# Kernel optimization log

Measured on AMD Instinct MI355X. Metric: run time of the kernel, lower is better.

The kernel has to match this reference:

```python
import jax, jax.numpy as jnp
import numpy as np

INPUT_DIM = 1024
HIDDEN_DIM = 2048
NUM_BLOCKS = 8
BLOCK_SIZE = HIDDEN_DIM // NUM_BLOCKS
BATCH = 2048


def setup_inputs() -> dict:
    key = jax.random.key(0)
    ks = jax.random.split(key, 6)
    # PyTorch GRUCell init: uniform(-1/sqrt(hidden_size), 1/sqrt(hidden_size))
    bound = 1.0 / np.sqrt(BLOCK_SIZE)
    u = lambda k, shape: jax.random.uniform(k, shape, jnp.float32, -bound, bound)
    return {
        "input": jax.random.normal(ks[0], (BATCH, INPUT_DIM), jnp.float32),
        "hidden": jax.random.normal(ks[1], (BATCH, HIDDEN_DIM), jnp.float32),
        # stacked per-block GRUCell params (block-diagonal structure)
        "W_ih": u(ks[2], (NUM_BLOCKS, 3 * BLOCK_SIZE, INPUT_DIM)),
        "W_hh": u(ks[3], (NUM_BLOCKS, 3 * BLOCK_SIZE, BLOCK_SIZE)),
        "b_ih": u(ks[4], (NUM_BLOCKS, 3 * BLOCK_SIZE)),
        "b_hh": u(ks[5], (NUM_BLOCKS, 3 * BLOCK_SIZE)),
    }


def reference(input, hidden, W_ih, W_hh, b_ih, b_hh):
    B = input.shape[0]
    nb, g3, bs = W_hh.shape  # [num_blocks, 3*block_size, block_size]
    hb = hidden.reshape(B, nb, bs)                      # [B, nb, bs]
    # input-to-gate and hidden-to-gate projections, batched over blocks
    gi = jnp.einsum("bi,ngi->bng", input, W_ih) + b_ih  # [B, nb, 3*bs]
    gh = jnp.einsum("bns,ngs->bng", hb, W_hh) + b_hh    # [B, nb, 3*bs]
    i_r, i_z, i_n = jnp.split(gi, 3, axis=-1)
    h_r, h_z, h_n = jnp.split(gh, 3, axis=-1)
    r = jax.nn.sigmoid(i_r + h_r)
    z = jax.nn.sigmoid(i_z + h_z)
    n = jnp.tanh(i_n + r * h_n)
    new_h = (1.0 - z) * n + z * hb                      # [B, nb, bs]
    return new_h.reshape(B, nb * bs)
```

## Files before the change

kernel.cpp:

```cpp
#include <hip/hip_runtime.h>
#include <hip/hip_bf16.h>
#include <type_traits>

typedef __attribute__((ext_vector_type(4))) float f32x4;
typedef __attribute__((ext_vector_type(8))) short bf16x8;

static constexpr int B_   = 2048;
static constexpr int IN_  = 1024;
static constexpr int HID_ = 2048;
static constexpr int NB_  = 8;
static constexpr int BS_  = 256;
static constexpr int G3_  = 768;

__device__ __forceinline__ unsigned cvtpk(float lo, float hi) {
  unsigned r;
  asm("v_cvt_pk_bf16_f32 %0, %1, %2" : "=v"(r) : "v"(lo), "v"(hi));
  return r;
}

__global__ __launch_bounds__(256, 2) void gru_mfma(
    const float* __restrict__ xf,
    const float* __restrict__ hf,
    const float* __restrict__ Wih,
    const float* __restrict__ Whh,
    const float* __restrict__ b_ih,
    const float* __restrict__ b_hh,
    float* __restrict__ out)
{
  __shared__ __align__(16) char lds[2][20480];

  const int t    = threadIdx.x;
  const int lane = t & 63;
  const int wid  = t >> 6;
  const int wm   = wid >> 1;
  const int wn   = wid & 1;

  const int bid = blockIdx.x;
  const int swz = (bid & 7) * 64 + (bid >> 3);
  const int mrow0 = (swz & 15) * 128;
  const int ct    = swz >> 4;
  const int n     = ct >> 2;
  const int s0    = (ct & 3) * 64;

  int arow[2], acolE[2];
#pragma unroll
  for (int p = 0; p < 2; ++p) {
    int op = p * 4096 + t * 16;
    int sx = ((op >> 6) & 3) ^ ((op >> 8) & 3);
    int ol = op ^ (sx << 4);
    arow[p]  = ol >> 6;
    acolE[p] = (ol & 63) >> 1;
  }
  int wgrow[3], wcolE[3];
#pragma unroll
  for (int q = 0; q < 3; ++q) {
    int op = q * 4096 + t * 16;
    int sx = ((op >> 6) & 3) ^ ((op >> 8) & 3);
    int ol = op ^ (sx << 4);
    int wr = ol >> 6;
    wgrow[q]  = n * G3_ + (wr >> 6) * BS_ + s0 + (wr & 63);
    wcolE[q]  = (ol & 63) >> 1;
  }

  f32x4 acc[4][4][2] = {};
  float4 sa[2][2];
  float4 sw[3][2];

  auto issue = [&](int tt) {
#pragma unroll
    for (int p = 0; p < 2; ++p) {
      const float* src = (tt < 32)
        ? xf + (size_t)(mrow0 + arow[p]) * IN_  + tt * 32 + acolE[p]
        : hf + (size_t)(mrow0 + arow[p]) * HID_ + n * BS_ + (tt - 32) * 32 + acolE[p];
      sa[p][0] = *reinterpret_cast<const float4*>(src);
      sa[p][1] = *reinterpret_cast<const float4*>(src + 4);
    }
#pragma unroll
    for (int q = 0; q < 3; ++q) {
      const float* src = (tt < 32)
        ? Wih + (size_t)wgrow[q] * IN_ + tt * 32 + wcolE[q]
        : Whh + (size_t)wgrow[q] * BS_ + (tt - 32) * 32 + wcolE[q];
      sw[q][0] = *reinterpret_cast<const float4*>(src);
      sw[q][1] = *reinterpret_cast<const float4*>(src + 4);
    }
  };
  auto pack8 = [&](const float4& a, const float4& b) {
    union { unsigned u[4]; bf16x8 v; } r;
    r.u[0] = cvtpk(a.x, a.y); r.u[1] = cvtpk(a.z, a.w);
    r.u[2] = cvtpk(b.x, b.y); r.u[3] = cvtpk(b.z, b.w);
    return r.v;
  };
  auto writeAll = [&](int buf) {
    char* base = (char*)lds[buf];
#pragma unroll
    for (int p = 0; p < 2; ++p)
      *reinterpret_cast<bf16x8*>(base + p * 4096 + t * 16) = pack8(sa[p][0], sa[p][1]);
#pragma unroll
    for (int q = 0; q < 3; ++q)
      *reinterpret_cast<bf16x8*>(base + 8192 + q * 4096 + t * 16) = pack8(sw[q][0], sw[q][1]);
  };

  auto compute = [&](int buf, auto ph1c) {
    constexpr bool PH1 = decltype(ph1c)::value;
    const char* base = (const char*)lds[buf];
    bf16x8 af[4];
#pragma unroll
    for (int mi = 0; mi < 4; ++mi) {
      int ar = wm * 64 + mi * 16 + (lane & 15);
      int sg = (ar & 3) ^ ((ar >> 2) & 3);
      int off = ar * 64 + ((((lane >> 4)) ^ sg) << 4);
      af[mi] = *reinterpret_cast<const bf16x8*>(base + off);
    }
    __builtin_amdgcn_s_setprio(1);
#pragma unroll
    for (int g = 0; g < 3; ++g) {
      bf16x8 wf[2];
#pragma unroll
      for (int ni = 0; ni < 2; ++ni) {
        int wr = g * 64 + wn * 32 + ni * 16 + (lane & 15);
        int sg = (wr & 3) ^ ((wr >> 2) & 3);
        int off = wr * 64 + ((((lane >> 4)) ^ sg) << 4);
        wf[ni] = *reinterpret_cast<const bf16x8*>(base + 8192 + off);
      }
      constexpr int set2 = PH1 ? 2 : 3;
      const int set = (g < 2) ? g : set2;
#pragma unroll
      for (int mi = 0; mi < 4; ++mi)
#pragma unroll
        for (int ni = 0; ni < 2; ++ni)
          acc[set][mi][ni] = __builtin_amdgcn_mfma_f32_16x16x32_bf16(
              af[mi], wf[ni], acc[set][mi][ni], 0, 0, 0);
    }
    __builtin_amdgcn_s_setprio(0);
  };

  issue(0);
  writeAll(0);
  __syncthreads();

#pragma unroll
  for (int tt = 0; tt < 40; ++tt) {
    const int cur = tt & 1;

    if (tt < 39) issue(tt + 1);
    __builtin_amdgcn_sched_barrier(0);
    if (tt < 32) compute(cur, std::true_type{});
    else         compute(cur, std::false_type{});
    __builtin_amdgcn_sched_barrier(0);
    if (tt < 39) writeAll(cur ^ 1);
    __syncthreads();
  }

  float* ew = (float*)lds + wid * 2304;
  const int gc0 = n * BS_ + s0 + wn * 32;

#pragma unroll
  for (int half = 0; half < 2; ++half) {
#pragma unroll
    for (int ml = 0; ml < 2; ++ml) {
      const int mi = half * 2 + ml;
#pragma unroll
      for (int ni = 0; ni < 2; ++ni) {
        int scol = s0 + wn * 32 + ni * 16 + (lane & 15);
        float br_i = b_ih[n * G3_ + 0 * BS_ + scol];
        float bz_i = b_ih[n * G3_ + 1 * BS_ + scol];
        float bn_i = b_ih[n * G3_ + 2 * BS_ + scol];
        float br_h = b_hh[n * G3_ + 0 * BS_ + scol];
        float bz_h = b_hh[n * G3_ + 1 * BS_ + scol];
        float bn_h = b_hh[n * G3_ + 2 * BS_ + scol];
#pragma unroll
        for (int i = 0; i < 4; ++i) {
          float rr = acc[0][mi][ni][i] + br_i + br_h;
          float zz = acc[1][mi][ni][i] + bz_i + bz_h;
          float r  = 1.f / (1.f + __expf(-rr));
          float z  = 1.f / (1.f + __expf(-zz));
          float ng = tanhf(acc[2][mi][ni][i] + bn_i + r * (acc[3][mi][ni][i] + bn_h));
          int lrow = ml * 16 + (lane >> 4) * 4 + i;
          int lcol = ni * 16 + (lane & 15);
          ew[lrow * 72 + lcol]      = z;
          ew[lrow * 72 + 36 + lcol] = ng;
        }
      }
    }
    asm volatile("s_waitcnt lgkmcnt(0)");
    __builtin_amdgcn_sched_barrier(0);
#pragma unroll
    for (int p = 0; p < 4; ++p) {
      int lrow = p * 8 + (lane >> 3);
      int grow = mrow0 + wm * 64 + half * 32 + lrow;
      int cc   = (lane & 7) * 4;
      float4 z4  = *reinterpret_cast<const float4*>(ew + lrow * 72 + cc);
      float4 ng4 = *reinterpret_cast<const float4*>(ew + lrow * 72 + 36 + cc);
      float4 h4  = *reinterpret_cast<const float4*>(hf + (size_t)grow * HID_ + gc0 + cc);
      float4 o4;
      o4.x = (1.f - z4.x) * ng4.x + z4.x * h4.x;
      o4.y = (1.f - z4.y) * ng4.y + z4.y * h4.y;
      o4.z = (1.f - z4.z) * ng4.z + z4.z * h4.z;
      o4.w = (1.f - z4.w) * ng4.w + z4.w * h4.w;
      *reinterpret_cast<float4*>(out + (size_t)grow * HID_ + gc0 + cc) = o4;
    }
    if (half == 0) {
      asm volatile("s_waitcnt lgkmcnt(0)");
      __builtin_amdgcn_sched_barrier(0);
    }
  }
}

extern "C" void kernel_launch(void* const* d_in, const int* in_sizes, int n_in,
                              void* d_out, int out_size, void* d_ws, size_t ws_size,
                              hipStream_t stream) {
  const float* x   = (const float*)d_in[0];
  const float* h   = (const float*)d_in[1];
  const float* Wih = (const float*)d_in[2];
  const float* Whh = (const float*)d_in[3];
  const float* bih = (const float*)d_in[4];
  const float* bhh = (const float*)d_in[5];
  float* out = (float*)d_out;
  (void)d_ws; (void)ws_size;

  gru_mfma<<<512, 256, 0, stream>>>(x, h, Wih, Whh, bih, bhh, out);
}
```

Measured before the change: 52.83 us.

## Halve M tile to 64 rows, double grid, switch LDS to padded layout

Each workgroup now covers 64 batch rows instead of 128, so the grid doubles to 1024 blocks and the accumulator count per thread halves. Launch bounds rise to 3 workgroups per CU. The XOR-swizzled LDS layout is replaced by an 80-byte padded row stride to avoid bank conflicts, and the epilogue is reshaped to match. This trades more occupancy and better CU balance for more weight traffic per output, since each weight tile is now reused across fewer rows.

Result: slower. 78.46 us (+48.5%).

```diff
diff --git a/kernel.cpp b/kernel.cpp
--- a/kernel.cpp
+++ b/kernel.cpp
@@ -18,7 +18,7 @@
   return r;
 }
 
-__global__ __launch_bounds__(256, 2) void gru_mfma(
+__global__ __launch_bounds__(256, 3) void gru_mfma(
     const float* __restrict__ xf,
     const float* __restrict__ hf,
     const float* __restrict__ Wih,
@@ -36,50 +36,40 @@
   const int wn   = wid & 1;
 
   const int bid = blockIdx.x;
-  const int swz = (bid & 7) * 64 + (bid >> 3);
-  const int mrow0 = (swz & 15) * 128;
-  const int ct    = swz >> 4;
+  const int swz = (bid & 7) * 128 + (bid >> 3);
+  const int mrow0 = (swz & 31) * 64;
+  const int ct    = swz >> 5;
   const int n     = ct >> 2;
   const int s0    = (ct & 3) * 64;
 
-  int arow[2], acolE[2];
-#pragma unroll
-  for (int p = 0; p < 2; ++p) {
-    int op = p * 4096 + t * 16;
-    int sx = ((op >> 6) & 3) ^ ((op >> 8) & 3);
-    int ol = op ^ (sx << 4);
-    arow[p]  = ol >> 6;
-    acolE[p] = (ol & 63) >> 1;
+  const int ar_  = t >> 2;
+  const int ac_  = (t & 3) * 8;
+  int wrow[3], wgrow[3], wcE[3];
+#pragma unroll
+  for (int q = 0; q < 3; ++q) {
+    int j = q * 256 + t;
+    wrow[q]  = j >> 2;
+    wcE[q]   = (j & 3) * 8;
+    wgrow[q] = n * G3_ + (wrow[q] >> 6) * BS_ + s0 + (wrow[q] & 63);
   }
-  int wgrow[3], wcolE[3];
-#pragma unroll
-  for (int q = 0; q < 3; ++q) {
-    int op = q * 4096 + t * 16;
-    int sx = ((op >> 6) & 3) ^ ((op >> 8) & 3);
-    int ol = op ^ (sx << 4);
-    int wr = ol >> 6;
-    wgrow[q]  = n * G3_ + (wr >> 6) * BS_ + s0 + (wr & 63);
-    wcolE[q]  = (ol & 63) >> 1;
-  }
-
-  f32x4 acc[4][4][2] = {};
-  float4 sa[2][2];
+
+  f32x4 acc[4][2][2] = {};
+  float4 sa[2];
   float4 sw[3][2];
 
   auto issue = [&](int tt) {
-#pragma unroll
-    for (int p = 0; p < 2; ++p) {
+    {
       const float* src = (tt < 32)
-        ? xf + (size_t)(mrow0 + arow[p]) * IN_  + tt * 32 + acolE[p]
-        : hf + (size_t)(mrow0 + arow[p]) * HID_ + n * BS_ + (tt - 32) * 32 + acolE[p];
-      sa[p][0] = *reinterpret_cast<const float4*>(src);
-      sa[p][1] = *reinterpret_cast<const float4*>(src + 4);
+        ? xf + (size_t)(mrow0 + ar_) * IN_  + tt * 32 + ac_
+        : hf + (size_t)(mrow0 + ar_) * HID_ + n * BS_ + (tt - 32) * 32 + ac_;
+      sa[0] = *reinterpret_cast<const float4*>(src);
+      sa[1] = *reinterpret_cast<const float4*>(src + 4);
     }
 #pragma unroll
     for (int q = 0; q < 3; ++q) {
       const float* src = (tt < 32)
-        ? Wih + (size_t)wgrow[q] * IN_ + tt * 32 + wcolE[q]
-        : Whh + (size_t)wgrow[q] * BS_ + (tt - 32) * 32 + wcolE[q];
+        ? Wih + (size_t)wgrow[q] * IN_ + tt * 32 + wcE[q]
+        : Whh + (size_t)wgrow[q] * BS_ + (tt - 32) * 32 + wcE[q];
       sw[q][0] = *reinterpret_cast<const float4*>(src);
       sw[q][1] = *reinterpret_cast<const float4*>(src + 4);
     }
@@ -92,24 +82,21 @@
   };
   auto writeAll = [&](int buf) {
     char* base = (char*)lds[buf];
-#pragma unroll
-    for (int p = 0; p < 2; ++p)
-      *reinterpret_cast<bf16x8*>(base + p * 4096 + t * 16) = pack8(sa[p][0], sa[p][1]);
+    *reinterpret_cast<bf16x8*>(base + ar_ * 80 + (t & 3) * 16) = pack8(sa[0], sa[1]);
 #pragma unroll
     for (int q = 0; q < 3; ++q)
-      *reinterpret_cast<bf16x8*>(base + 8192 + q * 4096 + t * 16) = pack8(sw[q][0], sw[q][1]);
+      *reinterpret_cast<bf16x8*>(base + 5120 + wrow[q] * 80 + ((q * 256 + t) & 3) * 16)
+          = pack8(sw[q][0], sw[q][1]);
   };
 
   auto compute = [&](int buf, auto ph1c) {
     constexpr bool PH1 = decltype(ph1c)::value;
     const char* base = (const char*)lds[buf];
-    bf16x8 af[4];
-#pragma unroll
-    for (int mi = 0; mi < 4; ++mi) {
-      int ar = wm * 64 + mi * 16 + (lane & 15);
-      int sg = (ar & 3) ^ ((ar >> 2) & 3);
-      int off = ar * 64 + ((((lane >> 4)) ^ sg) << 4);
-      af[mi] = *reinterpret_cast<const bf16x8*>(base + off);
+    bf16x8 af[2];
+#pragma unroll
+    for (int mi = 0; mi < 2; ++mi) {
+      int r = wm * 32 + mi * 16 + (lane & 15);
+      af[mi] = *reinterpret_cast<const bf16x8*>(base + r * 80 + ((lane >> 4) * 16));
     }
     __builtin_amdgcn_s_setprio(1);
 #pragma unroll
@@ -118,14 +105,12 @@
 #pragma unroll
       for (int ni = 0; ni < 2; ++ni) {
         int wr = g * 64 + wn * 32 + ni * 16 + (lane & 15);
-        int sg = (wr & 3) ^ ((wr >> 2) & 3);
-        int off = wr * 64 + ((((lane >> 4)) ^ sg) << 4);
-        wf[ni] = *reinterpret_cast<const bf16x8*>(base + 8192 + off);
+        wf[ni] = *reinterpret_cast<const bf16x8*>(base + 5120 + wr * 80 + ((lane >> 4) * 16));
       }
       constexpr int set2 = PH1 ? 2 : 3;
       const int set = (g < 2) ? g : set2;
 #pragma unroll
-      for (int mi = 0; mi < 4; ++mi)
+      for (int mi = 0; mi < 2; ++mi)
 #pragma unroll
         for (int ni = 0; ni < 2; ++ni)
           acc[set][mi][ni] = __builtin_amdgcn_mfma_f32_16x16x32_bf16(
@@ -141,7 +126,6 @@
 #pragma unroll
   for (int tt = 0; tt < 40; ++tt) {
     const int cur = tt & 1;
-
     if (tt < 39) issue(tt + 1);
     __builtin_amdgcn_sched_barrier(0);
     if (tt < 32) compute(cur, std::true_type{});
@@ -151,46 +135,42 @@
     __syncthreads();
   }
 
-  float* ew = (float*)lds + wid * 2304;
+  float* ew = (float*)lds + wid * 1152;
   const int gc0 = n * BS_ + s0 + wn * 32;
 
 #pragma unroll
-  for (int half = 0; half < 2; ++half) {
-#pragma unroll
-    for (int ml = 0; ml < 2; ++ml) {
-      const int mi = half * 2 + ml;
-#pragma unroll
-      for (int ni = 0; ni < 2; ++ni) {
-        int scol = s0 + wn * 32 + ni * 16 + (lane & 15);
-        float br_i = b_ih[n * G3_ + 0 * BS_ + scol];
-        float bz_i = b_ih[n * G3_ + 1 * BS_ + scol];
-        float bn_i = b_ih[n * G3_ + 2 * BS_ + scol];
-        float br_h = b_hh[n * G3_ + 0 * BS_ + scol];
-        float bz_h = b_hh[n * G3_ + 1 * BS_ + scol];
-        float bn_h = b_hh[n * G3_ + 2 * BS_ + scol];
-#pragma unroll
-        for (int i = 0; i < 4; ++i) {
-          float rr = acc[0][mi][ni][i] + br_i + br_h;
-          float zz = acc[1][mi][ni][i] + bz_i + bz_h;
-          float r  = 1.f / (1.f + __expf(-rr));
-          float z  = 1.f / (1.f + __expf(-zz));
-          float ng = tanhf(acc[2][mi][ni][i] + bn_i + r * (acc[3][mi][ni][i] + bn_h));
-          int lrow = ml * 16 + (lane >> 4) * 4 + i;
-          int lcol = ni * 16 + (lane & 15);
-          ew[lrow * 72 + lcol]      = z;
-          ew[lrow * 72 + 36 + lcol] = ng;
-        }
+  for (int mi = 0; mi < 2; ++mi) {
+#pragma unroll
+    for (int ni = 0; ni < 2; ++ni) {
+      int scol = s0 + wn * 32 + ni * 16 + (lane & 15);
+      float br_i = b_ih[n * G3_ + 0 * BS_ + scol];
+      float bz_i = b_ih[n * G3_ + 1 * BS_ + scol];
+      float bn_i = b_ih[n * G3_ + 2 * BS_ + scol];
+      float br_h = b_hh[n * G3_ + 0 * BS_ + scol];
+      float bz_h = b_hh[n * G3_ + 1 * BS_ + scol];
+      float bn_h = b_hh[n * G3_ + 2 * BS_ + scol];
+#pragma unroll
+      for (int i = 0; i < 4; ++i) {
+        float rr = acc[0][mi][ni][i] + br_i + br_h;
+        float zz = acc[1][mi][ni][i] + bz_i + bz_h;
+        float r  = 1.f / (1.f + __expf(-rr));
+        float z  = 1.f / (1.f + __expf(-zz));
+        float ng = tanhf(acc[2][mi][ni][i] + bn_i + r * (acc[3][mi][ni][i] + bn_h));
+        int lrow = (lane >> 4) * 4 + i;
+        int lcol = ni * 16 + (lane & 15);
+        ew[lrow * 36 + lcol]       = z;
+        ew[576 + lrow * 36 + lcol] = ng;
       }
     }
     asm volatile("s_waitcnt lgkmcnt(0)");
     __builtin_amdgcn_sched_barrier(0);
 #pragma unroll
-    for (int p = 0; p < 4; ++p) {
+    for (int p = 0; p < 2; ++p) {
       int lrow = p * 8 + (lane >> 3);
-      int grow = mrow0 + wm * 64 + half * 32 + lrow;
+      int grow = mrow0 + wm * 32 + mi * 16 + lrow;
       int cc   = (lane & 7) * 4;
-      float4 z4  = *reinterpret_cast<const float4*>(ew + lrow * 72 + cc);
-      float4 ng4 = *reinterpret_cast<const float4*>(ew + lrow * 72 + 36 + cc);
+      float4 z4  = *reinterpret_cast<const float4*>(ew + lrow * 36 + cc);
+      float4 ng4 = *reinterpret_cast<const float4*>(ew + 576 + lrow * 36 + cc);
       float4 h4  = *reinterpret_cast<const float4*>(hf + (size_t)grow * HID_ + gc0 + cc);
       float4 o4;
       o4.x = (1.f - z4.x) * ng4.x + z4.x * h4.x;
@@ -199,7 +179,7 @@
       o4.w = (1.f - z4.w) * ng4.w + z4.w * h4.w;
       *reinterpret_cast<float4*>(out + (size_t)grow * HID_ + gc0 + cc) = o4;
     }
-    if (half == 0) {
+    if (mi == 0) {
       asm volatile("s_waitcnt lgkmcnt(0)");
       __builtin_amdgcn_sched_barrier(0);
     }
@@ -218,5 +198,5 @@
   float* out = (float*)d_out;
   (void)d_ws; (void)ws_size;
 
-  gru_mfma<<<512, 256, 0, stream>>>(x, h, Wih, Whh, bih, bhh, out);
+  gru_mfma<<<1024, 256, 0, stream>>>(x, h, Wih, Whh, bih, bhh, out);
 }
```
